# Kernel tuning notes

Hardware: AMD Instinct MI355X
Metric: run time of the kernel (lower is better)

## Reference

```python
import jax, jax.numpy as jnp
import numpy as np

HEADS = 8
CPH = 32


def _rel_pos_indices(h, w):
    # same construction as the torch buffer, done statically in numpy
    coords = np.stack(np.meshgrid(np.arange(h), np.arange(w), indexing='ij')).reshape(2, -1)  # [2, N]
    rel = coords[:, :, None] - coords[:, None, :]  # [2, N, N]
    idx = (rel[0] + h - 1) * (2 * w - 1) + (rel[1] + w - 1)  # [N, N]
    return jnp.asarray(idx, dtype=jnp.int32)


def setup_inputs() -> dict:
    key = jax.random.key(0)
    ks = jax.random.split(key, 6)
    B, C, H, W = 2, 256, 48, 48
    emb = HEADS * CPH  # 256
    x = jax.random.normal(ks[0], (B, C, H, W), dtype=jnp.float32)
    # GDN params (kept positive so sqrt is well-defined)
    gdn_beta = jnp.ones((C,), dtype=jnp.float32)
    gdn_gamma = 0.1 * jnp.eye(C, dtype=jnp.float32) + 0.001 * jax.random.uniform(ks[1], (C, C), dtype=jnp.float32)
    w_qkv = 0.02 * jax.random.normal(ks[2], (3 * emb, C), dtype=jnp.float32)
    w_out = 0.02 * jax.random.normal(ks[3], (C, emb), dtype=jnp.float32)
    b_out = jnp.zeros((C,), dtype=jnp.float32)
    table_size = (2 * H - 1) * (2 * W - 1)
    rel_bias_table = 0.02 * jax.random.normal(ks[4], (table_size, HEADS), dtype=jnp.float32)
    return {"x": x, "gdn_beta": gdn_beta, "gdn_gamma": gdn_gamma,
            "w_qkv": w_qkv, "w_out": w_out, "b_out": b_out,
            "rel_bias_table": rel_bias_table}


def reference(x, gdn_beta, gdn_gamma, w_qkv, w_out, b_out, rel_bias_table):
    B, C, H, W = x.shape
    N = H * W
    emb = HEADS * CPH
    scale = CPH ** (-0.5)

    # GDN: y = x / sqrt(beta + gamma * x^2)  (1x1 conv over channels of x^2)
    norm = jnp.einsum('bchw,dc->bdhw', x * x, gdn_gamma) + gdn_beta[None, :, None, None]
    xn = x / jnp.sqrt(norm)

    # flatten spatial, channels last: [B, N, C]
    t = xn.reshape(B, C, N).transpose(0, 2, 1)

    # qkv projection (no bias)
    qkv = (t @ w_qkv.T).reshape(B, N, 3, HEADS, CPH).transpose(2, 0, 3, 1, 4)  # [3, B, h, N, d]
    q, k, v = qkv[0], qkv[1], qkv[2]

    attn = jnp.einsum('bhnd,bhmd->bhnm', q, k) * scale  # [B, h, N, N]

    # gathered relative position bias: [h, N, N]
    idx = _rel_pos_indices(H, W)  # [N, N], static ints
    bias = rel_bias_table[idx.reshape(-1)].reshape(N, N, HEADS).transpose(2, 0, 1)
    attn = jax.nn.softmax(attn + bias[None], axis=-1)

    # NOTE: faithful to the original quirk — reshape (B, h, N, d) directly
    # to (B, N, C) with NO head/seq transpose, exactly like the torch code.
    res = jnp.einsum('bhnm,bhmd->bhnd', attn, v).reshape(B, N, emb)

    out = res @ w_out.T + b_out  # [B, N, C]
    return out.transpose(0, 2, 1).reshape(B, C, H, W)
```

## Files before the change

### kernel.cpp

```cpp
#include <hip/hip_runtime.h>
#include <cstdint>
#include <cstddef>

typedef __attribute__((ext_vector_type(8))) short short8;
typedef __attribute__((ext_vector_type(4))) float floatx4;
typedef __attribute__((ext_vector_type(4))) unsigned short ushort4v;

#define NB 2
#define NPIX 2304
#define TBL 9025
#define TBLP 9032
#define L2E 1.4426950408889634f
#define QSCALE 0.17677669529663689f
#define NTILES 36

__device__ __forceinline__ float b2f(unsigned short u) {
  union { unsigned int i; float f; } v; v.i = ((unsigned int)u) << 16; return v.f;
}
__device__ __forceinline__ float bits2f(unsigned int i) {
  union { unsigned int i; float f; } v; v.i = i; return v.f;
}
__device__ __forceinline__ unsigned short f2b(float f) {
  union { float f; unsigned int i; } v; v.f = f;
  return (unsigned short)((v.i + 0x7fffu + ((v.i >> 16) & 1u)) >> 16);
}
__device__ __forceinline__ unsigned int cvtpk(float lo, float hi) {
  unsigned int r;
  asm("v_cvt_pk_bf16_f32 %0, %1, %2" : "=v"(r) : "v"(lo), "v"(hi));
  return r;
}

__global__ __launch_bounds__(256) void prep_k(
    const float* __restrict__ gamma, const float* __restrict__ wqkv,
    const float* __restrict__ wout, const float* __restrict__ table,
    unsigned short* __restrict__ gb, unsigned short* __restrict__ qb,
    unsigned short* __restrict__ wb, unsigned short* __restrict__ tb)
{
  int i = blockIdx.x * 256 + threadIdx.x;
  if (i < 65536)  gb[i] = f2b(gamma[i]);
  if (i < 196608) qb[i] = f2b(wqkv[i]);
  if (i < 65536)  wb[i] = f2b(wout[i]);
  if (i < TBL * 8) {
    int e = i >> 3, h = i & 7;
    tb[(size_t)h * TBLP + e] = f2b(table[i] * L2E);
  }
}

template<int MODE>
__global__ __launch_bounds__(256) void gemm_k(
    const unsigned short* __restrict__ A,
    const void* __restrict__ Bv,
    const float* __restrict__ vec,
    unsigned short* __restrict__ o0,
    unsigned short* __restrict__ o1,
    unsigned short* __restrict__ o2,
    float* __restrict__ of)
{
  __shared__ unsigned short Al[64][40];
  __shared__ unsigned short Bl[64][40];
  const float* __restrict__ X = (const float*)Bv;
  const unsigned short* __restrict__ Bw = (const unsigned short*)Bv;

  const int n0 = blockIdx.x * 64;
  const int m0 = blockIdx.y * 64;
  const int b  = blockIdx.z;
  const int tid = threadIdx.x;
  const int wave = tid >> 6, lane = tid & 63;
  const int wm = wave >> 1, wn = wave & 1;
  const int lm = lane & 15, quad = lane >> 4;

  const int ml = tid >> 2, ko = (tid & 3) * 8;
  const int kkB = tid >> 3, n8 = (tid & 7) * 8;
  const int nl = tid >> 2;

  short8 areg = *(const short8*)&A[(size_t)(m0 + ml) * 256 + ko];
  short8 bregs;
  float4 bx0, bx1;
  if (MODE == 0) {
    const float* xr = &X[((size_t)(b * 256 + kkB)) * NPIX + n0 + n8];
    bx0 = *(const float4*)xr;
    bx1 = *(const float4*)(xr + 4);
  } else {
    bregs = *(const short8*)&Bw[((size_t)b * NPIX + n0 + nl) * 256 + ko];
  }

  floatx4 acc[2][2] = {};

  for (int k0 = 0; k0 < 256; k0 += 32) {
    __syncthreads();
    *(short8*)&Al[ml][ko] = areg;
    if (MODE == 0) {
      Bl[n8 + 0][kkB] = f2b(bx0.x * bx0.x);
      Bl[n8 + 1][kkB] = f2b(bx0.y * bx0.y);
      Bl[n8 + 2][kkB] = f2b(bx0.z * bx0.z);
      Bl[n8 + 3][kkB] = f2b(bx0.w * bx0.w);
      Bl[n8 + 4][kkB] = f2b(bx1.x * bx1.x);
      Bl[n8 + 5][kkB] = f2b(bx1.y * bx1.y);
      Bl[n8 + 6][kkB] = f2b(bx1.z * bx1.z);
      Bl[n8 + 7][kkB] = f2b(bx1.w * bx1.w);
    } else {
      *(short8*)&Bl[nl][ko] = bregs;
    }
    __syncthreads();

    if (k0 + 32 < 256) {
      areg = *(const short8*)&A[(size_t)(m0 + ml) * 256 + (k0 + 32) + ko];
      if (MODE == 0) {
        const float* xr = &X[((size_t)(b * 256 + (k0 + 32) + kkB)) * NPIX + n0 + n8];
        bx0 = *(const float4*)xr;
        bx1 = *(const float4*)(xr + 4);
      } else {
        bregs = *(const short8*)&Bw[((size_t)b * NPIX + n0 + nl) * 256 + (k0 + 32) + ko];
      }
    }

    short8 af[2], bfr[2];
    #pragma unroll
    for (int tm = 0; tm < 2; ++tm)
      af[tm] = *(const short8*)&Al[wm*32 + tm*16 + lm][quad*8];
    #pragma unroll
    for (int tn = 0; tn < 2; ++tn)
      bfr[tn] = *(const short8*)&Bl[wn*32 + tn*16 + lm][quad*8];
    #pragma unroll
    for (int tm = 0; tm < 2; ++tm)
      #pragma unroll
      for (int tn = 0; tn < 2; ++tn)
        acc[tm][tn] = __builtin_amdgcn_mfma_f32_16x16x32_bf16(af[tm], bfr[tn], acc[tm][tn], 0, 0, 0);
  }

  #pragma unroll
  for (int tm = 0; tm < 2; ++tm) {
    const int rbase = m0 + wm*32 + tm*16 + quad*4;
    #pragma unroll
    for (int tn = 0; tn < 2; ++tn) {
      const int col = n0 + wn*32 + tn*16 + lm;
      floatx4 a4 = acc[tm][tn];
      if (MODE == 0) {
        ushort4v pk;
        #pragma unroll
        for (int r = 0; r < 4; ++r) {
          int d = rbase + r;
          float xv = X[((size_t)(b * 256 + d)) * NPIX + col];
          pk[r] = f2b(xv * rsqrtf(vec[d] + a4[r]));
        }
        *(ushort4v*)&o0[((size_t)(b * NPIX + col)) * 256 + rbase] = pk;
      } else if (MODE == 1) {
        const int part = rbase >> 8, h = (rbase >> 5) & 7, dd = rbase & 31;
        if (part == 2) {
          #pragma unroll
          for (int r = 0; r < 4; ++r)
            o2[(((size_t)(b * 8 + h)) * 32 + dd + r) * NPIX + col] = f2b(a4[r]);
        } else {
          unsigned short* dst = part == 0 ? o0 : o1;
          const float sc = (part == 0) ? (QSCALE * L2E) : 1.0f;
          ushort4v pk;
          #pragma unroll
          for (int r = 0; r < 4; ++r) pk[r] = f2b(a4[r] * sc);
          *(ushort4v*)&dst[(((size_t)(b * 8 + h)) * NPIX + col) * 32 + dd] = pk;
        }
      } else {
        #pragma unroll
        for (int r = 0; r < 4; ++r) {
          int c = rbase + r;
          of[((size_t)(b * 256 + c)) * NPIX + col] = a4[r] + vec[c];
        }
      }
    }
  }
}

__global__ __launch_bounds__(576) void attn_k(
    const unsigned short* __restrict__ qg, const unsigned short* __restrict__ kg,
    const unsigned short* __restrict__ vt, const unsigned short* __restrict__ tabt,
    unsigned short* __restrict__ ob)
{
  __shared__ __align__(16) unsigned short tab[TBLP];
  __shared__ __align__(16) unsigned short Pl[9][16][72];

  const int tid = threadIdx.x;
  const int w = tid >> 6, lane = tid & 63;
  const int lm = lane & 15, quad = lane >> 4;
  const int bh = blockIdx.x;
  const int q0 = blockIdx.y * 144;
  const size_t base = (size_t)bh * NPIX * 32;

  {
    const unsigned short* src = tabt + (size_t)(bh & 7) * TBLP;
    for (int e = tid * 8; e < TBLP; e += 4608)
      *(short8*)&tab[e] = *(const short8*)&src[e];
  }
  __syncthreads();

  const int q = q0 + w * 16 + lm;
  const short8 qfrag = *(const short8*)&qg[base + (size_t)q * 32 + quad * 8];

  const int hi = (q * 43691) >> 21;
  const int rb = (hi + 47) * 95 + (q - hi * 48) + 47;

  const unsigned short* pk0 = kg + base + (size_t)lm * 32 + quad * 8;
  const unsigned short* pv0 = vt + base + (size_t)lm * NPIX + quad * 8;

  float lsum = 0.f;
  floatx4 o[2] = {};

  for (int t = 0; t < NTILES; ++t) {
    const int j0 = t * 64;
    floatx4 s4[4];
    #pragma unroll
    for (int kt = 0; kt < 4; ++kt) {
      short8 kf = *(const short8*)(pk0 + kt * 512);
      floatx4 z = {};
      s4[kt] = __builtin_amdgcn_mfma_f32_16x16x32_bf16(kf, qfrag, z, 0, 0, 0);
    }
    #pragma unroll
    for (int kt = 0; kt < 4; ++kt) {
      const int kk = j0 + kt * 16 + quad * 4;
      const int hj = (kk * 43691) >> 21;
      const int bb = rb - kk - hj * 47;
      uint2 bv;
      __builtin_memcpy(&bv, &tab[bb - 3], 8);
      float p0 = __builtin_amdgcn_exp2f(s4[kt][0] + bits2f(bv.y & 0xFFFF0000u));
      float p1 = __builtin_amdgcn_exp2f(s4[kt][1] + bits2f(bv.y << 16));
      float p2 = __builtin_amdgcn_exp2f(s4[kt][2] + bits2f(bv.x & 0xFFFF0000u));
      float p3 = __builtin_amdgcn_exp2f(s4[kt][3] + bits2f(bv.x << 16));
      lsum += (p0 + p1) + (p2 + p3);
      uint2 pk = { cvtpk(p0, p1), cvtpk(p2, p3) };
      *(uint2*)&Pl[w][lm][kt * 16 + quad * 4] = pk;
    }
    __asm__ volatile("s_waitcnt lgkmcnt(0)" ::: "memory");
    #pragma unroll
    for (int c = 0; c < 2; ++c) {
      short8 pf = *(const short8*)&Pl[w][lm][c * 32 + quad * 8];
      #pragma unroll
      for (int dt = 0; dt < 2; ++dt) {
        short8 vf = *(const short8*)(pv0 + dt * 16 * NPIX + c * 32);
        o[dt] = __builtin_amdgcn_mfma_f32_16x16x32_bf16(vf, pf, o[dt], 0, 0, 0);
      }
    }
    pk0 += 2048;
    pv0 += 64;
  }

  lsum += __shfl_xor(lsum, 16, 64);
  lsum += __shfl_xor(lsum, 32, 64);
  const float inv = 1.f / lsum;

  #pragma unroll
  for (int dt = 0; dt < 2; ++dt) {
    uint2 pk = { cvtpk(o[dt][0] * inv, o[dt][1] * inv),
                 cvtpk(o[dt][2] * inv, o[dt][3] * inv) };
    *(uint2*)&ob[base + (size_t)q * 32 + dt * 16 + quad * 4] = pk;
  }
}

extern "C" void kernel_launch(void* const* d_in, const int* in_sizes, int n_in,
                              void* d_out, int out_size, void* d_ws, size_t ws_size,
                              hipStream_t stream) {
  const float* x     = (const float*)d_in[0];
  const float* beta  = (const float*)d_in[1];
  const float* gamma = (const float*)d_in[2];
  const float* wqkv  = (const float*)d_in[3];
  const float* wout  = (const float*)d_in[4];
  const float* bout  = (const float*)d_in[5];
  const float* table = (const float*)d_in[6];
  float* out = (float*)d_out;

  unsigned short* ws = (unsigned short*)d_ws;
  const size_t NE = (size_t)NB * NPIX * 256;
  unsigned short* xn_t  = ws;
  unsigned short* qbuf  = ws + NE;
  unsigned short* kbuf  = ws + 2 * NE;
  unsigned short* vtbuf = ws + 3 * NE;
  unsigned short* obuf  = ws + 4 * NE;
  unsigned short* gam_b = obuf;
  unsigned short* qkv_b = obuf + 65536;
  unsigned short* out_b = ws + 5 * NE;
  unsigned short* tab_t = ws + 5 * NE + 65536;

  prep_k<<<768, 256, 0, stream>>>(gamma, wqkv, wout, table, gam_b, qkv_b, out_b, tab_t);
  gemm_k<0><<<dim3(36, 4, 2), 256, 0, stream>>>(gam_b, x, beta, xn_t, nullptr, nullptr, nullptr);
  gemm_k<1><<<dim3(36, 12, 2), 256, 0, stream>>>(qkv_b, xn_t, nullptr, qbuf, kbuf, vtbuf, nullptr);
  attn_k<<<dim3(16, 16), 576, 0, stream>>>(qbuf, kbuf, vtbuf, tab_t, obuf);
  gemm_k<2><<<dim3(36, 4, 2), 256, 0, stream>>>(out_b, obuf, bout, nullptr, nullptr, nullptr, out);
}
```

Before: 151.4 us.

## Transpose P fragment via ds_bpermute instead of LDS round-trip

Replaces the per-wave shared-memory staging of the softmax probability tile with in-register cross-lane shuffles (ds_bpermute) that rearrange the S accumulator layout into the B-operand layout for the PV MFMA. It also hoists the V fragment global loads ahead of the exp computation so their latency overlaps the softmax math. This removes LDS writes, an explicit lgkmcnt wait and LDS reads per tile, at the cost of eight bpermutes per 32-column chunk plus selects, and more live registers for the prefetched V.

```diff
diff --git a/kernel.cpp b/kernel.cpp
--- a/kernel.cpp
+++ b/kernel.cpp
@@ -175,11 +175,11 @@
     unsigned short* __restrict__ ob)
 {
   __shared__ __align__(16) unsigned short tab[TBLP];
-  __shared__ __align__(16) unsigned short Pl[9][16][72];
 
   const int tid = threadIdx.x;
-  const int w = tid >> 6, lane = tid & 63;
+  const int lane = tid & 63;
   const int lm = lane & 15, quad = lane >> 4;
+  const int w = tid >> 6;
   const int bh = blockIdx.x;
   const int q0 = blockIdx.y * 144;
   const size_t base = (size_t)bh * NPIX * 32;
@@ -200,6 +200,10 @@
   const unsigned short* pk0 = kg + base + (size_t)lm * 32 + quad * 8;
   const unsigned short* pv0 = vt + base + (size_t)lm * NPIX + quad * 8;
 
+  const int la4 = (lm + ((quad & 1) << 5)) << 2;
+  const int lb4 = la4 + 64;
+  const bool hsel = (quad & 2) != 0;
+
   float lsum = 0.f;
   floatx4 o[2] = {};
 
@@ -212,6 +216,14 @@
       floatx4 z = {};
       s4[kt] = __builtin_amdgcn_mfma_f32_16x16x32_bf16(kf, qfrag, z, 0, 0, 0);
     }
+    short8 vf[2][2];
+    #pragma unroll
+    for (int c = 0; c < 2; ++c)
+      #pragma unroll
+      for (int dt = 0; dt < 2; ++dt)
+        vf[c][dt] = *(const short8*)(pv0 + dt * 16 * NPIX + c * 32);
+
+    unsigned int pkx[4], pky[4];
     #pragma unroll
     for (int kt = 0; kt < 4; ++kt) {
       const int kk = j0 + kt * 16 + quad * 4;
@@ -224,18 +236,28 @@
       float p2 = __builtin_amdgcn_exp2f(s4[kt][2] + bits2f(bv.x & 0xFFFF0000u));
       float p3 = __builtin_amdgcn_exp2f(s4[kt][3] + bits2f(bv.x << 16));
       lsum += (p0 + p1) + (p2 + p3);
-      uint2 pk = { cvtpk(p0, p1), cvtpk(p2, p3) };
-      *(uint2*)&Pl[w][lm][kt * 16 + quad * 4] = pk;
-    }
-    __asm__ volatile("s_waitcnt lgkmcnt(0)" ::: "memory");
+      pkx[kt] = cvtpk(p0, p1);
+      pky[kt] = cvtpk(p2, p3);
+    }
+
     #pragma unroll
     for (int c = 0; c < 2; ++c) {
-      short8 pf = *(const short8*)&Pl[w][lm][c * 32 + quad * 8];
+      int a0 = __builtin_amdgcn_ds_bpermute(la4, (int)pkx[2*c]);
+      int b0 = __builtin_amdgcn_ds_bpermute(la4, (int)pkx[2*c+1]);
+      int a1 = __builtin_amdgcn_ds_bpermute(la4, (int)pky[2*c]);
+      int b1 = __builtin_amdgcn_ds_bpermute(la4, (int)pky[2*c+1]);
+      int a2 = __builtin_amdgcn_ds_bpermute(lb4, (int)pkx[2*c]);
+      int b2 = __builtin_amdgcn_ds_bpermute(lb4, (int)pkx[2*c+1]);
+      int a3 = __builtin_amdgcn_ds_bpermute(lb4, (int)pky[2*c]);
+      int b3 = __builtin_amdgcn_ds_bpermute(lb4, (int)pky[2*c+1]);
+      union { unsigned int u[4]; short8 s; } pf;
+      pf.u[0] = (unsigned int)(hsel ? b0 : a0);
+      pf.u[1] = (unsigned int)(hsel ? b1 : a1);
+      pf.u[2] = (unsigned int)(hsel ? b2 : a2);
+      pf.u[3] = (unsigned int)(hsel ? b3 : a3);
       #pragma unroll
-      for (int dt = 0; dt < 2; ++dt) {
-        short8 vf = *(const short8*)(pv0 + dt * 16 * NPIX + c * 32);
-        o[dt] = __builtin_amdgcn_mfma_f32_16x16x32_bf16(vf, pf, o[dt], 0, 0, 0);
-      }
+      for (int dt = 0; dt < 2; ++dt)
+        o[dt] = __builtin_amdgcn_mfma_f32_16x16x32_bf16(vf[c][dt], pf.s, o[dt], 0, 0, 0);
     }
     pk0 += 2048;
     pv0 += 64;
```

Measured after the change: 151.8 us. No clear change (+0.2%).
